# Kernel optimization log

Hardware: AMD Instinct MI355X
Metric: run time of the kernel (lower is better)

Reference implementation:

```python
import jax, jax.numpy as jnp
import numpy as np

N = 14           # num_wires
DEPTH = 2        # feature_map_depth; circuit applies DEPTH+1 StronglyEntanglingLayers blocks
SEL_LAYERS = 2   # params (B, 2*N*3) -> weights (B, 2, N, 3)


def _apply_1q(psi, U, w):
    # psi: (B, 2**N) complex64, U: (B,2,2) complex64, acts on wire w (wire 0 = MSB)
    B = psi.shape[0]
    psi = psi.reshape(B, 2 ** w, 2, -1)
    psi = jnp.einsum('bij,bajc->baic', U, psi)
    return psi.reshape(B, -1)


def _apply_cnot(psi, c, t):
    B = psi.shape[0]
    x = psi.reshape((B,) + (2,) * N)
    ca, ta = 1 + c, 1 + t
    a0 = jax.lax.index_in_dim(x, 0, ca, keepdims=True)
    a1 = jnp.flip(jax.lax.index_in_dim(x, 1, ca, keepdims=True), axis=ta)
    return jnp.concatenate([a0, a1], axis=ca).reshape(B, -1)


def _expz(psi, w):
    # <Z_w> = P(bit_w = 0) - P(bit_w = 1)
    B = psi.shape[0]
    p = (psi.real ** 2 + psi.imag ** 2).reshape(B, 2 ** w, 2, -1)
    return p[:, :, 0].sum(axis=(1, 2)) - p[:, :, 1].sum(axis=(1, 2))


def _rot(phi, theta, omega):
    # PennyLane Rot = RZ(omega) RY(theta) RZ(phi); returns (B,2,2) complex
    c, s = jnp.cos(theta / 2), jnp.sin(theta / 2)
    u00 = jnp.exp(-0.5j * (phi + omega)) * c
    u01 = -jnp.exp(0.5j * (phi - omega)) * s
    u10 = jnp.exp(-0.5j * (phi - omega)) * s
    u11 = jnp.exp(0.5j * (phi + omega)) * c
    return jnp.stack([jnp.stack([u00, u01], -1), jnp.stack([u10, u11], -1)], -2)


def _circuit(phases, weights):
    # phases: (B, N) float32, weights: (B, SEL_LAYERS, N, 3) float32
    B = phases.shape[0]
    psi = jnp.zeros((B, 2 ** N), jnp.complex64).at[:, 0].set(1.0)
    # AngleEmbedding (rotation='X'): RX(phi_w) on each wire
    for w in range(N):
        th = phases[:, w] / 2
        c, s = jnp.cos(th), jnp.sin(th)
        U = jnp.stack([jnp.stack([c + 0j, -1j * s], -1),
                       jnp.stack([-1j * s, c + 0j], -1)], -2)
        psi = _apply_1q(psi, U.astype(jnp.complex64), w)
    # (feature_map_depth + 1) StronglyEntanglingLayers blocks, all sharing `weights`
    for _ in range(DEPTH + 1):
        for l in range(SEL_LAYERS):
            for w in range(N):
                U = _rot(weights[:, l, w, 0], weights[:, l, w, 1], weights[:, l, w, 2])
                psi = _apply_1q(psi, U.astype(jnp.complex64), w)
            r = (l % (N - 1)) + 1  # PennyLane default ranges
            for w in range(N):
                psi = _apply_cnot(psi, w, (w + r) % N)
    return jnp.stack([_expz(psi, w) for w in range(N)], axis=1)  # (B, N)


def setup_inputs() -> dict:
    key = jax.random.key(0)
    k1, k2, k3, k4 = jax.random.split(key, 4)
    B = 512
    return {
        'state_batch': jax.random.normal(k1, (B, 2 ** N, 2), jnp.float32),
        'params': jax.random.normal(k2, (B, SEL_LAYERS * N * 3), jnp.float32),
        'head_w': jax.random.normal(k3, (1, N), jnp.float32) / np.float32(np.sqrt(N)),
        'head_b': jax.random.normal(k4, (1,), jnp.float32),
    }


def reference(state_batch, params, head_w, head_b):
    B = state_batch.shape[0]
    # torch.angle of a real tensor: pi where negative, 0 otherwise
    phases = jnp.where(state_batch.reshape(B, -1) < 0,
                       jnp.float32(np.pi), jnp.float32(0.0))[:, :N]
    weights = params.reshape(B, SEL_LAYERS, N, 3)
    qmeas = _circuit(phases, weights)            # (B, N)
    return (qmeas @ head_w.T + head_b)[:, 0]     # (B,)
```

## Files before the change

### kernel.cpp

```cpp
#include <hip/hip_runtime.h>


#define NW 14
#define NSTATE (1 << NW)
#define NTHREADS 1024
#define STATE_SLOTS (NSTATE + ((NSTATE >> 6) << 1))

__device__ __forceinline__ int SLOT(int i) { return i + ((i >> 6) << 1); }

typedef float v2f __attribute__((ext_vector_type(2)));

__device__ __forceinline__ float2 cmul(float2 a, float2 b) {
    return make_float2(a.x * b.x - a.y * b.y, a.x * b.y + a.y * b.x);
}

__device__ __forceinline__ v2f pk_mul_bl(v2f a, v2f b) {
    v2f d;
    asm("v_pk_mul_f32 %0, %1, %2 op_sel:[0,0] op_sel_hi:[1,0]"
        : "=v"(d) : "v"(a), "v"(b));
    return d;
}
__device__ __forceinline__ v2f pk_fma_bl(v2f a, v2f b, v2f c) {
    v2f d;
    asm("v_pk_fma_f32 %0, %1, %2, %3 op_sel:[0,0,0] op_sel_hi:[1,0,1]"
        : "=v"(d) : "v"(a), "v"(b), "v"(c));
    return d;
}
__device__ __forceinline__ v2f pk_fma_sw(v2f a, v2f b, v2f c) {
    v2f d;
    asm("v_pk_fma_f32 %0, %1, %2, %3 op_sel:[1,0,0] op_sel_hi:[0,1,1]"
        : "=v"(d) : "v"(a), "v"(b), "v"(c));
    return d;
}

struct RingConsts { unsigned col[2][NW]; unsigned flow[2][16]; };
constexpr RingConsts make_rc() {
    RingConsts rc{};
    for (int ri = 0; ri < 2; ++ri) {
        for (int bb = 0; bb < NW; ++bb) {
            unsigned x = 1u << bb;
            for (int w = 0; w < NW; ++w) {
                int pc = 13 - w, pt = 13 - ((w + ri + 1) % NW);
                x ^= ((x >> pc) & 1u) << pt;
            }
            rc.col[ri][bb] = x;
        }
        for (int k = 0; k < 16; ++k) {
            unsigned x = 0;
            for (int b = 0; b < 4; ++b) if ((k >> b) & 1) x ^= rc.col[ri][b];
            rc.flow[ri][k] = x;
        }
    }
    return rc;
}
constexpr RingConsts RC = make_rc();

#define GSTAGE(W) \
    const float4 g0 = G4[(W)*4+0], g1 = G4[(W)*4+1], \
                 g2 = G4[(W)*4+2], g3 = G4[(W)*4+3]; \
    const v2f U00 = (v2f){g0.x,g0.y}, V00 = (v2f){g0.z,g0.w}; \
    const v2f U01 = (v2f){g1.x,g1.y}, V01 = (v2f){g1.z,g1.w}; \
    const v2f U10 = (v2f){g2.x,g2.y}, V10 = (v2f){g2.z,g2.w}; \
    const v2f U11 = (v2f){g3.x,g3.y}, V11 = (v2f){g3.z,g3.w};

#define CBFA(X, Y) { \
    v2f n0 = pk_mul_bl(X, U00); n0 = pk_fma_sw(X, V00, n0); \
    n0 = pk_fma_bl(Y, U01, n0); n0 = pk_fma_sw(Y, V01, n0); \
    v2f n1 = pk_mul_bl(X, U10); n1 = pk_fma_sw(X, V10, n1); \
    n1 = pk_fma_bl(Y, U11, n1); n1 = pk_fma_sw(Y, V11, n1); \
    X = n0; Y = n1; }

template<int LO>
__device__ __forceinline__ void rot_pass(float2* st_, const float4* G4, int t)
{
    constexpr int S = (1 << LO) + ((LO >= 6) ? (1 << (LO - 5)) : 0);
    const int lowmask = (1 << LO) - 1;
    const int base = ((t >> LO) << (LO + 4)) | (t & lowmask);
    float2* p = st_ + SLOT(base);
    float2* q = p + 8 * S;
    v2f A0  = *(const v2f*)(p + 0*S), A1  = *(const v2f*)(p + 1*S),
        A2  = *(const v2f*)(p + 2*S), A3  = *(const v2f*)(p + 3*S),
        A4  = *(const v2f*)(p + 4*S), A5  = *(const v2f*)(p + 5*S),
        A6  = *(const v2f*)(p + 6*S), A7  = *(const v2f*)(p + 7*S),
        A8  = *(const v2f*)(q + 0*S), A9  = *(const v2f*)(q + 1*S),
        A10 = *(const v2f*)(q + 2*S), A11 = *(const v2f*)(q + 3*S),
        A12 = *(const v2f*)(q + 4*S), A13 = *(const v2f*)(q + 5*S),
        A14 = *(const v2f*)(q + 6*S), A15 = *(const v2f*)(q + 7*S);
    { GSTAGE(13 - LO - 3)
      CBFA(A0,A8) CBFA(A1,A9) CBFA(A2,A10) CBFA(A3,A11)
      CBFA(A4,A12) CBFA(A5,A13) CBFA(A6,A14) CBFA(A7,A15) }
    { GSTAGE(13 - LO - 2)
      CBFA(A0,A4) CBFA(A1,A5) CBFA(A2,A6) CBFA(A3,A7)
      CBFA(A8,A12) CBFA(A9,A13) CBFA(A10,A14) CBFA(A11,A15) }
    { GSTAGE(13 - LO - 1)
      CBFA(A0,A2) CBFA(A1,A3) CBFA(A4,A6) CBFA(A5,A7)
      CBFA(A8,A10) CBFA(A9,A11) CBFA(A12,A14) CBFA(A13,A15) }
    { GSTAGE(13 - LO)
      CBFA(A0,A1) CBFA(A2,A3) CBFA(A4,A5) CBFA(A6,A7)
      CBFA(A8,A9) CBFA(A10,A11) CBFA(A12,A13) CBFA(A14,A15) }
    *(v2f*)(p + 0*S) = A0;  *(v2f*)(p + 1*S) = A1;
    *(v2f*)(p + 2*S) = A2;  *(v2f*)(p + 3*S) = A3;
    *(v2f*)(p + 4*S) = A4;  *(v2f*)(p + 5*S) = A5;
    *(v2f*)(p + 6*S) = A6;  *(v2f*)(p + 7*S) = A7;
    *(v2f*)(q + 0*S) = A8;  *(v2f*)(q + 1*S) = A9;
    *(v2f*)(q + 2*S) = A10; *(v2f*)(q + 3*S) = A11;
    *(v2f*)(q + 4*S) = A12; *(v2f*)(q + 5*S) = A13;
    *(v2f*)(q + 6*S) = A14; *(v2f*)(q + 7*S) = A15;
}

#define LOW_LOAD_GATES \
    float2* pc = st_ + SLOT(t << 4); \
    const float4* lp = (const float4*)pc; \
    const float4 r0 = lp[0], r1 = lp[1], r2 = lp[2], r3 = lp[3], \
                 r4 = lp[4], r5 = lp[5], r6 = lp[6], r7 = lp[7]; \
    v2f A0  = (v2f){r0.x,r0.y}, A1  = (v2f){r0.z,r0.w}, \
        A2  = (v2f){r1.x,r1.y}, A3  = (v2f){r1.z,r1.w}, \
        A4  = (v2f){r2.x,r2.y}, A5  = (v2f){r2.z,r2.w}, \
        A6  = (v2f){r3.x,r3.y}, A7  = (v2f){r3.z,r3.w}, \
        A8  = (v2f){r4.x,r4.y}, A9  = (v2f){r4.z,r4.w}, \
        A10 = (v2f){r5.x,r5.y}, A11 = (v2f){r5.z,r5.w}, \
        A12 = (v2f){r6.x,r6.y}, A13 = (v2f){r6.z,r6.w}, \
        A14 = (v2f){r7.x,r7.y}, A15 = (v2f){r7.z,r7.w}; \
    { GSTAGE(12) \
      CBFA(A0,A2) CBFA(A1,A3) CBFA(A4,A6) CBFA(A5,A7) \
      CBFA(A8,A10) CBFA(A9,A11) CBFA(A12,A14) CBFA(A13,A15) } \
    { GSTAGE(13) \
      CBFA(A0,A1) CBFA(A2,A3) CBFA(A4,A5) CBFA(A6,A7) \
      CBFA(A8,A9) CBFA(A10,A11) CBFA(A12,A13) CBFA(A14,A15) }

template<int RI>
__device__ __forceinline__ void rot_low_ring(float2* st_, const float4* G4, int t,
                                             const unsigned* lutA_, const unsigned* lutB_)
{
    LOW_LOAD_GATES
    const unsigned fb = lutA_[t & 31] ^ lutB_[t >> 5];
    __syncthreads();
#define SCT(k, Ak) st_[SLOT((int)(fb ^ RC.flow[RI][k]))] = make_float2(Ak.x, Ak.y);
    SCT(0,A0) SCT(1,A1) SCT(2,A2) SCT(3,A3) SCT(4,A4) SCT(5,A5) SCT(6,A6) SCT(7,A7)
    SCT(8,A8) SCT(9,A9) SCT(10,A10) SCT(11,A11) SCT(12,A12) SCT(13,A13) SCT(14,A14) SCT(15,A15)
#undef SCT
}

__device__ __forceinline__ float rot_low_meas(float2* st_, const float4* G4, int t,
                                              const unsigned* lutA_, const unsigned* lutB_,
                                              const float* s_hw)
{
    LOW_LOAD_GATES
    const unsigned fb = lutA_[t & 31] ^ lutB_[t >> 5];
#define SGV(b) ((((fb >> b) & 1u) ? -1.f : 1.f) * s_hw[13 - (b)])
    const float sg0 = SGV(0),  sg1 = SGV(1),  sg2 = SGV(2),  sg3 = SGV(3),
                sg4 = SGV(4),  sg5 = SGV(5),  sg6 = SGV(6),  sg7 = SGV(7),
                sg8 = SGV(8),  sg9 = SGV(9),  sg10 = SGV(10), sg11 = SGV(11),
                sg12 = SGV(12), sg13 = SGV(13);
#undef SGV
    const float chiS = ((sg0 + sg1) + (sg2 + sg3)) + ((sg4 + sg5) + (sg6 + sg7))
                     + ((sg8 + sg9) + (sg10 + sg11)) + (sg12 + sg13);
#define SUBSUM(F) ( ((F)&1u?sg0:0.f) + ((F)&2u?sg1:0.f) + ((F)&4u?sg2:0.f) + ((F)&8u?sg3:0.f) \
                  + ((F)&16u?sg4:0.f) + ((F)&32u?sg5:0.f) + ((F)&64u?sg6:0.f) + ((F)&128u?sg7:0.f) \
                  + ((F)&256u?sg8:0.f) + ((F)&512u?sg9:0.f) + ((F)&1024u?sg10:0.f) + ((F)&2048u?sg11:0.f) \
                  + ((F)&4096u?sg12:0.f) + ((F)&8192u?sg13:0.f) )
    float acc = 0.f;
#define MEASA(k, Ak) { const float p2 = fmaf(Ak.x, Ak.x, Ak.y * Ak.y); \
    acc = fmaf(p2, chiS - 2.f * SUBSUM(RC.flow[1][k]), acc); }
    MEASA(0,A0) MEASA(1,A1) MEASA(2,A2) MEASA(3,A3)
    MEASA(4,A4) MEASA(5,A5) MEASA(6,A6) MEASA(7,A7)
    MEASA(8,A8) MEASA(9,A9) MEASA(10,A10) MEASA(11,A11)
    MEASA(12,A12) MEASA(13,A13) MEASA(14,A14) MEASA(15,A15)
#undef MEASA
#undef SUBSUM
    return acc;
}

__global__ __launch_bounds__(NTHREADS)
__attribute__((amdgpu_waves_per_eu(4, 4)))
void qsim(const float* __restrict__ sb, const float* __restrict__ pr,
          const float* __restrict__ hw, const float* __restrict__ hb,
          float* __restrict__ out)
{
    __shared__ __align__(16) float2 st[STATE_SLOTS];
    __shared__ __align__(16) float4 rotc[2][NW * 4];
    __shared__ unsigned lutA[2][32], lutB[2][32];
    __shared__ float s_hw[NW];
    __shared__ float s_red[NTHREADS / 64];
    __shared__ unsigned s_bmask;

    const int bid = blockIdx.x;
    const int t = threadIdx.x;

    if (t < 28) {
        int l = t / NW, w = t % NW;
        const float* p = pr + bid * 84 + l * 42 + w * 3;
        float phi = p[0], th = p[1], om = p[2];
        float s, cth;  __sincosf(0.5f * th, &s, &cth);
        float sa, ca, sd, cd;
        __sincosf(0.5f * (phi + om), &sa, &ca);
        __sincosf(0.5f * (phi - om), &sd, &cd);
        const float u00x = ca * cth, u00y = -sa * cth;
        const float u01x = -cd * s,  u01y = -sd * s;
        const float u10x = cd * s,   u10y = -sd * s;
        const float u11x = ca * cth, u11y = sa * cth;
        rotc[l][w*4+0] = make_float4(u00x, u00y, -u00y, u00y);
        rotc[l][w*4+1] = make_float4(u01x, u01y, -u01y, u01y);
        rotc[l][w*4+2] = make_float4(u10x, u10y, -u10y, u10y);
        rotc[l][w*4+3] = make_float4(u11x, u11y, -u11y, u11y);
    }
    if (t >= 64 && t < 192) {
        int j = t - 64, ri = j >> 6, tb = (j >> 5) & 1, m = j & 31;
        unsigned x = 0;
        for (int b = 0; b < 5; ++b)
            if ((m >> b) & 1) x ^= RC.col[ri][(tb ? 9 : 4) + b];
        if (tb) lutB[ri][m] = x; else lutA[ri][m] = x;
    }
    if (t >= 192 && t < 206) s_hw[t - 192] = hw[t - 192];
    if (t == 224) {
        const float* row = sb + (size_t)bid * (NSTATE * 2);
        unsigned m = 0;
        for (int w = 0; w < NW; ++w) m |= (row[w] < 0.0f ? 1u : 0u) << (13 - w);
        s_bmask = m;
    }
    __syncthreads();

    {
        const unsigned bm = s_bmask;
        float2 ph = make_float2(1.f, 0.f);
#pragma unroll
        for (int w = 0; w < 10; ++w) {
            int v = (t >> (9 - w)) & 1;
            int bw = (bm >> (13 - w)) & 1;
            float4 e = rotc[0][w*4 + v*2 + bw];
            ph = cmul(ph, make_float2(e.x, e.y));
        }
        const unsigned fb = lutA[0][t & 31] ^ lutB[0][t >> 5];
#pragma unroll
        for (int k = 0; k < 16; ++k) {
            float4 e3 = rotc[0][10*4 + (((k >> 3) & 1) * 2) + ((bm >> 3) & 1)];
            float4 e2 = rotc[0][11*4 + (((k >> 2) & 1) * 2) + ((bm >> 2) & 1)];
            float4 e1 = rotc[0][12*4 + (((k >> 1) & 1) * 2) + ((bm >> 1) & 1)];
            float4 e0 = rotc[0][13*4 + ((k & 1) * 2) + (bm & 1)];
            float2 pl = cmul(cmul(make_float2(e3.x, e3.y), make_float2(e2.x, e2.y)),
                             cmul(make_float2(e1.x, e1.y), make_float2(e0.x, e0.y)));
            st[SLOT((int)(fb ^ RC.flow[0][k]))] = cmul(ph, pl);
        }
    }
    __syncthreads();

#pragma unroll 1
    for (int rep = 0; rep < 4; ++rep) {
        const int l = (rep & 1) ? 0 : 1;
        const float4* G4 = &rotc[l][0];
        rot_pass<10>(st, G4, t); __syncthreads();
        rot_pass<6>(st, G4, t);  __syncthreads();
        rot_pass<2>(st, G4, t);  __syncthreads();
        if (l) rot_low_ring<1>(st, G4, t, lutA[1], lutB[1]);
        else   rot_low_ring<0>(st, G4, t, lutA[0], lutB[0]);
        __syncthreads();
    }
    rot_pass<10>(st, &rotc[1][0], t); __syncthreads();
    rot_pass<6>(st, &rotc[1][0], t); __syncthreads();
    rot_pass<2>(st, &rotc[1][0], t); __syncthreads();
    float acc = rot_low_meas(st, &rotc[1][0], t, lutA[1], lutB[1], s_hw);

    for (int off = 32; off > 0; off >>= 1) acc += __shfl_down(acc, off);
    if ((t & 63) == 0) s_red[t >> 6] = acc;
    __syncthreads();
    if (t == 0) {
        float tot = 0.f;
#pragma unroll
        for (int i = 0; i < NTHREADS / 64; ++i) tot += s_red[i];
        out[bid] = tot + hb[0];
    }
}

extern "C" void kernel_launch(void* const* d_in, const int* in_sizes, int n_in,
                              void* d_out, int out_size, void* d_ws, size_t ws_size,
                              hipStream_t stream)
{
    const float* sb = (const float*)d_in[0];
    const float* pr = (const float*)d_in[1];
    const float* hw = (const float*)d_in[2];
    const float* hb = (const float*)d_in[3];
    float* out = (float*)d_out;
    const int B = in_sizes[1] / 84;
    qsim<<<B, NTHREADS, 0, stream>>>(sb, pr, hw, hb, out);
}
```

Measured before the change: 208.9 us.

## Process 32 amplitudes per thread with 512 threads to cut LDS passes

After: 196.6 us. 5.9% less time.

```diff
diff --git a/kernel.cpp b/kernel.cpp
--- a/kernel.cpp
+++ b/kernel.cpp
@@ -3,10 +3,8 @@
 
 #define NW 14
 #define NSTATE (1 << NW)
-#define NTHREADS 1024
+#define NTHREADS 512
 #define STATE_SLOTS (NSTATE + ((NSTATE >> 6) << 1))
-
-__device__ __forceinline__ int SLOT(int i) { return i + ((i >> 6) << 1); }
 
 typedef float v2f __attribute__((ext_vector_type(2)));
 
@@ -15,25 +13,19 @@
 }
 
 __device__ __forceinline__ v2f pk_mul_bl(v2f a, v2f b) {
-    v2f d;
-    asm("v_pk_mul_f32 %0, %1, %2 op_sel:[0,0] op_sel_hi:[1,0]"
-        : "=v"(d) : "v"(a), "v"(b));
-    return d;
+    v2f d; asm("v_pk_mul_f32 %0, %1, %2 op_sel:[0,0] op_sel_hi:[1,0]"
+               : "=v"(d) : "v"(a), "v"(b)); return d;
 }
 __device__ __forceinline__ v2f pk_fma_bl(v2f a, v2f b, v2f c) {
-    v2f d;
-    asm("v_pk_fma_f32 %0, %1, %2, %3 op_sel:[0,0,0] op_sel_hi:[1,0,1]"
-        : "=v"(d) : "v"(a), "v"(b), "v"(c));
-    return d;
+    v2f d; asm("v_pk_fma_f32 %0, %1, %2, %3 op_sel:[0,0,0] op_sel_hi:[1,0,1]"
+               : "=v"(d) : "v"(a), "v"(b), "v"(c)); return d;
 }
 __device__ __forceinline__ v2f pk_fma_sw(v2f a, v2f b, v2f c) {
-    v2f d;
-    asm("v_pk_fma_f32 %0, %1, %2, %3 op_sel:[1,0,0] op_sel_hi:[0,1,1]"
-        : "=v"(d) : "v"(a), "v"(b), "v"(c));
-    return d;
-}
-
-struct RingConsts { unsigned col[2][NW]; unsigned flow[2][16]; };
+    v2f d; asm("v_pk_fma_f32 %0, %1, %2, %3 op_sel:[1,0,0] op_sel_hi:[0,1,1]"
+               : "=v"(d) : "v"(a), "v"(b), "v"(c)); return d;
+}
+
+struct RingConsts { unsigned col[2][NW]; unsigned flow[2][32]; };
 constexpr RingConsts make_rc() {
     RingConsts rc{};
     for (int ri = 0; ri < 2; ++ri) {
@@ -45,9 +37,9 @@
             }
             rc.col[ri][bb] = x;
         }
-        for (int k = 0; k < 16; ++k) {
+        for (int k = 0; k < 32; ++k) {
             unsigned x = 0;
-            for (int b = 0; b < 4; ++b) if ((k >> b) & 1) x ^= rc.col[ri][b];
+            for (int b = 0; b < 5; ++b) if ((k >> b) & 1) x ^= rc.col[ri][b];
             rc.flow[ri][k] = x;
         }
     }
@@ -70,83 +62,93 @@
     n1 = pk_fma_bl(Y, U11, n1); n1 = pk_fma_sw(Y, V11, n1); \
     X = n0; Y = n1; }
 
-template<int LO>
-__device__ __forceinline__ void rot_pass(float2* st_, const float4* G4, int t)
-{
-    constexpr int S = (1 << LO) + ((LO >= 6) ? (1 << (LO - 5)) : 0);
-    const int lowmask = (1 << LO) - 1;
-    const int base = ((t >> LO) << (LO + 4)) | (t & lowmask);
-    float2* p = st_ + SLOT(base);
-    float2* q = p + 8 * S;
-    v2f A0  = *(const v2f*)(p + 0*S), A1  = *(const v2f*)(p + 1*S),
-        A2  = *(const v2f*)(p + 2*S), A3  = *(const v2f*)(p + 3*S),
-        A4  = *(const v2f*)(p + 4*S), A5  = *(const v2f*)(p + 5*S),
-        A6  = *(const v2f*)(p + 6*S), A7  = *(const v2f*)(p + 7*S),
-        A8  = *(const v2f*)(q + 0*S), A9  = *(const v2f*)(q + 1*S),
-        A10 = *(const v2f*)(q + 2*S), A11 = *(const v2f*)(q + 3*S),
-        A12 = *(const v2f*)(q + 4*S), A13 = *(const v2f*)(q + 5*S),
-        A14 = *(const v2f*)(q + 6*S), A15 = *(const v2f*)(q + 7*S);
-    { GSTAGE(13 - LO - 3)
-      CBFA(A0,A8) CBFA(A1,A9) CBFA(A2,A10) CBFA(A3,A11)
-      CBFA(A4,A12) CBFA(A5,A13) CBFA(A6,A14) CBFA(A7,A15) }
-    { GSTAGE(13 - LO - 2)
-      CBFA(A0,A4) CBFA(A1,A5) CBFA(A2,A6) CBFA(A3,A7)
-      CBFA(A8,A12) CBFA(A9,A13) CBFA(A10,A14) CBFA(A11,A15) }
-    { GSTAGE(13 - LO - 1)
-      CBFA(A0,A2) CBFA(A1,A3) CBFA(A4,A6) CBFA(A5,A7)
-      CBFA(A8,A10) CBFA(A9,A11) CBFA(A12,A14) CBFA(A13,A15) }
-    { GSTAGE(13 - LO)
-      CBFA(A0,A1) CBFA(A2,A3) CBFA(A4,A5) CBFA(A6,A7)
-      CBFA(A8,A9) CBFA(A10,A11) CBFA(A12,A13) CBFA(A14,A15) }
-    *(v2f*)(p + 0*S) = A0;  *(v2f*)(p + 1*S) = A1;
-    *(v2f*)(p + 2*S) = A2;  *(v2f*)(p + 3*S) = A3;
-    *(v2f*)(p + 4*S) = A4;  *(v2f*)(p + 5*S) = A5;
-    *(v2f*)(p + 6*S) = A6;  *(v2f*)(p + 7*S) = A7;
-    *(v2f*)(q + 0*S) = A8;  *(v2f*)(q + 1*S) = A9;
-    *(v2f*)(q + 2*S) = A10; *(v2f*)(q + 3*S) = A11;
-    *(v2f*)(q + 4*S) = A12; *(v2f*)(q + 5*S) = A13;
-    *(v2f*)(q + 6*S) = A14; *(v2f*)(q + 7*S) = A15;
+#define FE32(M) M(0) M(1) M(2) M(3) M(4) M(5) M(6) M(7) M(8) M(9) M(10) M(11) \
+    M(12) M(13) M(14) M(15) M(16) M(17) M(18) M(19) M(20) M(21) M(22) M(23) \
+    M(24) M(25) M(26) M(27) M(28) M(29) M(30) M(31)
+
+#define P4(M) M(A0,A16) M(A1,A17) M(A2,A18) M(A3,A19) M(A4,A20) M(A5,A21) M(A6,A22) M(A7,A23) \
+              M(A8,A24) M(A9,A25) M(A10,A26) M(A11,A27) M(A12,A28) M(A13,A29) M(A14,A30) M(A15,A31)
+#define P3(M) M(A0,A8) M(A1,A9) M(A2,A10) M(A3,A11) M(A4,A12) M(A5,A13) M(A6,A14) M(A7,A15) \
+              M(A16,A24) M(A17,A25) M(A18,A26) M(A19,A27) M(A20,A28) M(A21,A29) M(A22,A30) M(A23,A31)
+#define P2(M) M(A0,A4) M(A1,A5) M(A2,A6) M(A3,A7) M(A8,A12) M(A9,A13) M(A10,A14) M(A11,A15) \
+              M(A16,A20) M(A17,A21) M(A18,A22) M(A19,A23) M(A24,A28) M(A25,A29) M(A26,A30) M(A27,A31)
+#define P1(M) M(A0,A2) M(A1,A3) M(A4,A6) M(A5,A7) M(A8,A10) M(A9,A11) M(A12,A14) M(A13,A15) \
+              M(A16,A18) M(A17,A19) M(A20,A22) M(A21,A23) M(A24,A26) M(A25,A27) M(A28,A30) M(A29,A31)
+#define P0(M) M(A0,A1) M(A2,A3) M(A4,A5) M(A6,A7) M(A8,A9) M(A10,A11) M(A12,A13) M(A14,A15) \
+              M(A16,A17) M(A18,A19) M(A20,A21) M(A22,A23) M(A24,A25) M(A26,A27) M(A28,A29) M(A30,A31)
+
+template<int LO, int W0>
+__device__ __forceinline__ void rot_pass5(float2* st_, const float4* G4, int t)
+{
+    const int base = ((t >> LO) << (LO + 5)) | (t & ((1 << LO) - 1));
+    float2* pA = st_ + (base + ((base >> 6) << 1));
+#define OFF(k) ((((k)) << LO) + (((((k)) << LO) >> 6) << 1))
+    float2* pB = pA + OFF(16);
+#define ADR(k) ((k) < 16 ? (pA + OFF(k)) : (pB + OFF((k) - 16)))
+#define DECL(k) v2f A##k;
+    FE32(DECL)
+#undef DECL
+#define LD(k) A##k = *(const v2f*)ADR(k);
+    FE32(LD)
+#undef LD
+    { GSTAGE(W0+0) P4(CBFA) }
+    { GSTAGE(W0+1) P3(CBFA) }
+    { GSTAGE(W0+2) P2(CBFA) }
+    { GSTAGE(W0+3) P1(CBFA) }
+    { GSTAGE(W0+4) P0(CBFA) }
+#define ST(k) *(v2f*)ADR(k) = A##k;
+    FE32(ST)
+#undef ST
+#undef ADR
+#undef OFF
 }
 
 #define LOW_LOAD_GATES \
-    float2* pc = st_ + SLOT(t << 4); \
-    const float4* lp = (const float4*)pc; \
-    const float4 r0 = lp[0], r1 = lp[1], r2 = lp[2], r3 = lp[3], \
-                 r4 = lp[4], r5 = lp[5], r6 = lp[6], r7 = lp[7]; \
-    v2f A0  = (v2f){r0.x,r0.y}, A1  = (v2f){r0.z,r0.w}, \
-        A2  = (v2f){r1.x,r1.y}, A3  = (v2f){r1.z,r1.w}, \
-        A4  = (v2f){r2.x,r2.y}, A5  = (v2f){r2.z,r2.w}, \
-        A6  = (v2f){r3.x,r3.y}, A7  = (v2f){r3.z,r3.w}, \
-        A8  = (v2f){r4.x,r4.y}, A9  = (v2f){r4.z,r4.w}, \
-        A10 = (v2f){r5.x,r5.y}, A11 = (v2f){r5.z,r5.w}, \
-        A12 = (v2f){r6.x,r6.y}, A13 = (v2f){r6.z,r6.w}, \
-        A14 = (v2f){r7.x,r7.y}, A15 = (v2f){r7.z,r7.w}; \
-    { GSTAGE(12) \
-      CBFA(A0,A2) CBFA(A1,A3) CBFA(A4,A6) CBFA(A5,A7) \
-      CBFA(A8,A10) CBFA(A9,A11) CBFA(A12,A14) CBFA(A13,A15) } \
-    { GSTAGE(13) \
-      CBFA(A0,A1) CBFA(A2,A3) CBFA(A4,A5) CBFA(A6,A7) \
-      CBFA(A8,A9) CBFA(A10,A11) CBFA(A12,A13) CBFA(A14,A15) }
+    const float4* lp = (const float4*)(st_ + (32 * t + ((t >> 1) << 1))); \
+    const float4 q0 = lp[0],  q1 = lp[1],  q2 = lp[2],  q3 = lp[3], \
+                 q4 = lp[4],  q5 = lp[5],  q6 = lp[6],  q7 = lp[7], \
+                 q8 = lp[8],  q9 = lp[9],  q10 = lp[10], q11 = lp[11], \
+                 q12 = lp[12], q13 = lp[13], q14 = lp[14], q15 = lp[15]; \
+    v2f A0  = (v2f){q0.x,q0.y},  A1  = (v2f){q0.z,q0.w}, \
+        A2  = (v2f){q1.x,q1.y},  A3  = (v2f){q1.z,q1.w}, \
+        A4  = (v2f){q2.x,q2.y},  A5  = (v2f){q2.z,q2.w}, \
+        A6  = (v2f){q3.x,q3.y},  A7  = (v2f){q3.z,q3.w}, \
+        A8  = (v2f){q4.x,q4.y},  A9  = (v2f){q4.z,q4.w}, \
+        A10 = (v2f){q5.x,q5.y},  A11 = (v2f){q5.z,q5.w}, \
+        A12 = (v2f){q6.x,q6.y},  A13 = (v2f){q6.z,q6.w}, \
+        A14 = (v2f){q7.x,q7.y},  A15 = (v2f){q7.z,q7.w}, \
+        A16 = (v2f){q8.x,q8.y},  A17 = (v2f){q8.z,q8.w}, \
+        A18 = (v2f){q9.x,q9.y},  A19 = (v2f){q9.z,q9.w}, \
+        A20 = (v2f){q10.x,q10.y}, A21 = (v2f){q10.z,q10.w}, \
+        A22 = (v2f){q11.x,q11.y}, A23 = (v2f){q11.z,q11.w}, \
+        A24 = (v2f){q12.x,q12.y}, A25 = (v2f){q12.z,q12.w}, \
+        A26 = (v2f){q13.x,q13.y}, A27 = (v2f){q13.z,q13.w}, \
+        A28 = (v2f){q14.x,q14.y}, A29 = (v2f){q14.z,q14.w}, \
+        A30 = (v2f){q15.x,q15.y}, A31 = (v2f){q15.z,q15.w}; \
+    { GSTAGE(10) P3(CBFA) } \
+    { GSTAGE(11) P2(CBFA) } \
+    { GSTAGE(12) P1(CBFA) } \
+    { GSTAGE(13) P0(CBFA) }
 
 template<int RI>
-__device__ __forceinline__ void rot_low_ring(float2* st_, const float4* G4, int t,
-                                             const unsigned* lutA_, const unsigned* lutB_)
+__device__ __forceinline__ void rot_low_ring5(float2* st_, const float4* G4, int t,
+                                              const unsigned* lA, const unsigned* lB)
 {
     LOW_LOAD_GATES
-    const unsigned fb = lutA_[t & 31] ^ lutB_[t >> 5];
-    __syncthreads();
-#define SCT(k, Ak) st_[SLOT((int)(fb ^ RC.flow[RI][k]))] = make_float2(Ak.x, Ak.y);
-    SCT(0,A0) SCT(1,A1) SCT(2,A2) SCT(3,A3) SCT(4,A4) SCT(5,A5) SCT(6,A6) SCT(7,A7)
-    SCT(8,A8) SCT(9,A9) SCT(10,A10) SCT(11,A11) SCT(12,A12) SCT(13,A13) SCT(14,A14) SCT(15,A15)
-#undef SCT
-}
-
-__device__ __forceinline__ float rot_low_meas(float2* st_, const float4* G4, int t,
-                                              const unsigned* lutA_, const unsigned* lutB_,
-                                              const float* s_hw)
+    const unsigned fb = lA[t & 31] ^ lB[t >> 5];
+    __syncthreads();
+#define SC(k) { const unsigned ix = fb ^ RC.flow[RI][(k)]; \
+    st_[ix + ((ix >> 6) << 1)] = make_float2(A##k.x, A##k.y); }
+    FE32(SC)
+#undef SC
+}
+
+__device__ __forceinline__ float rot_low_meas5(float2* st_, const float4* G4, int t,
+                                               const unsigned* lA, const unsigned* lB,
+                                               const float* s_hw)
 {
     LOW_LOAD_GATES
-    const unsigned fb = lutA_[t & 31] ^ lutB_[t >> 5];
+    const unsigned fb = lA[t & 31] ^ lB[t >> 5];
 #define SGV(b) ((((fb >> b) & 1u) ? -1.f : 1.f) * s_hw[13 - (b)])
     const float sg0 = SGV(0),  sg1 = SGV(1),  sg2 = SGV(2),  sg3 = SGV(3),
                 sg4 = SGV(4),  sg5 = SGV(5),  sg6 = SGV(6),  sg7 = SGV(7),
@@ -160,26 +162,23 @@
                   + ((F)&256u?sg8:0.f) + ((F)&512u?sg9:0.f) + ((F)&1024u?sg10:0.f) + ((F)&2048u?sg11:0.f) \
                   + ((F)&4096u?sg12:0.f) + ((F)&8192u?sg13:0.f) )
     float acc = 0.f;
-#define MEASA(k, Ak) { const float p2 = fmaf(Ak.x, Ak.x, Ak.y * Ak.y); \
-    acc = fmaf(p2, chiS - 2.f * SUBSUM(RC.flow[1][k]), acc); }
-    MEASA(0,A0) MEASA(1,A1) MEASA(2,A2) MEASA(3,A3)
-    MEASA(4,A4) MEASA(5,A5) MEASA(6,A6) MEASA(7,A7)
-    MEASA(8,A8) MEASA(9,A9) MEASA(10,A10) MEASA(11,A11)
-    MEASA(12,A12) MEASA(13,A13) MEASA(14,A14) MEASA(15,A15)
-#undef MEASA
+#define MEASK(k) { const float p2 = fmaf(A##k.x, A##k.x, A##k.y * A##k.y); \
+    acc = fmaf(p2, chiS - 2.f * SUBSUM(RC.flow[1][(k)]), acc); }
+    FE32(MEASK)
+#undef MEASK
 #undef SUBSUM
     return acc;
 }
 
-__global__ __launch_bounds__(NTHREADS)
-__attribute__((amdgpu_waves_per_eu(4, 4)))
+__global__ __launch_bounds__(NTHREADS, 2)
 void qsim(const float* __restrict__ sb, const float* __restrict__ pr,
           const float* __restrict__ hw, const float* __restrict__ hb,
           float* __restrict__ out)
 {
     __shared__ __align__(16) float2 st[STATE_SLOTS];
     __shared__ __align__(16) float4 rotc[2][NW * 4];
-    __shared__ unsigned lutA[2][32], lutB[2][32];
+    __shared__ unsigned lutA[2][32], lutB[2][16];
+    __shared__ float2 low_tab[32];
     __shared__ float s_hw[NW];
     __shared__ float s_red[NTHREADS / 64];
     __shared__ unsigned s_bmask;
@@ -204,43 +203,55 @@
         rotc[l][w*4+2] = make_float4(u10x, u10y, -u10y, u10y);
         rotc[l][w*4+3] = make_float4(u11x, u11y, -u11y, u11y);
     }
-    if (t >= 64 && t < 192) {
-        int j = t - 64, ri = j >> 6, tb = (j >> 5) & 1, m = j & 31;
+    if (t >= 64 && t < 128) {
+        int j = t - 64, ri = j >> 5, m = j & 31;
         unsigned x = 0;
-        for (int b = 0; b < 5; ++b)
-            if ((m >> b) & 1) x ^= RC.col[ri][(tb ? 9 : 4) + b];
-        if (tb) lutB[ri][m] = x; else lutA[ri][m] = x;
-    }
-    if (t >= 192 && t < 206) s_hw[t - 192] = hw[t - 192];
-    if (t == 224) {
+        for (int b = 0; b < 5; ++b) if ((m >> b) & 1) x ^= RC.col[ri][5 + b];
+        lutA[ri][m] = x;
+    }
+    if (t >= 128 && t < 160) {
+        int j = t - 128, ri = j >> 4, m = j & 15;
+        unsigned x = 0;
+        for (int b = 0; b < 4; ++b) if ((m >> b) & 1) x ^= RC.col[ri][10 + b];
+        lutB[ri][m] = x;
+    }
+    if (t >= 160 && t < 174) s_hw[t - 160] = hw[t - 160];
+    if (t == 192) {
         const float* row = sb + (size_t)bid * (NSTATE * 2);
         unsigned m = 0;
         for (int w = 0; w < NW; ++w) m |= (row[w] < 0.0f ? 1u : 0u) << (13 - w);
         s_bmask = m;
     }
     __syncthreads();
+    if (t < 32) {
+        const unsigned bm = s_bmask;
+        float2 v = make_float2(1.f, 0.f);
+#pragma unroll
+        for (int b = 0; b < 5; ++b) {
+            int w = 13 - b, kb = (t >> b) & 1, cb = (bm >> b) & 1;
+            float4 e = rotc[0][w*4 + kb*2 + cb];
+            v = cmul(v, make_float2(e.x, e.y));
+        }
+        low_tab[t] = v;
+    }
+    __syncthreads();
 
     {
         const unsigned bm = s_bmask;
         float2 ph = make_float2(1.f, 0.f);
 #pragma unroll
-        for (int w = 0; w < 10; ++w) {
-            int v = (t >> (9 - w)) & 1;
+        for (int w = 0; w < 9; ++w) {
+            int v = (t >> (8 - w)) & 1;
             int bw = (bm >> (13 - w)) & 1;
             float4 e = rotc[0][w*4 + v*2 + bw];
             ph = cmul(ph, make_float2(e.x, e.y));
         }
         const unsigned fb = lutA[0][t & 31] ^ lutB[0][t >> 5];
-#pragma unroll
-        for (int k = 0; k < 16; ++k) {
-            float4 e3 = rotc[0][10*4 + (((k >> 3) & 1) * 2) + ((bm >> 3) & 1)];
-            float4 e2 = rotc[0][11*4 + (((k >> 2) & 1) * 2) + ((bm >> 2) & 1)];
-            float4 e1 = rotc[0][12*4 + (((k >> 1) & 1) * 2) + ((bm >> 1) & 1)];
-            float4 e0 = rotc[0][13*4 + ((k & 1) * 2) + (bm & 1)];
-            float2 pl = cmul(cmul(make_float2(e3.x, e3.y), make_float2(e2.x, e2.y)),
-                             cmul(make_float2(e1.x, e1.y), make_float2(e0.x, e0.y)));
-            st[SLOT((int)(fb ^ RC.flow[0][k]))] = cmul(ph, pl);
-        }
+#define INITK(k) { const unsigned ix = fb ^ RC.flow[0][(k)]; \
+    const float2 lt = low_tab[(k)]; \
+    st[ix + ((ix >> 6) << 1)] = cmul(ph, lt); }
+        FE32(INITK)
+#undef INITK
     }
     __syncthreads();
 
@@ -248,17 +259,15 @@
     for (int rep = 0; rep < 4; ++rep) {
         const int l = (rep & 1) ? 0 : 1;
         const float4* G4 = &rotc[l][0];
-        rot_pass<10>(st, G4, t); __syncthreads();
-        rot_pass<6>(st, G4, t);  __syncthreads();
-        rot_pass<2>(st, G4, t);  __syncthreads();
-        if (l) rot_low_ring<1>(st, G4, t, lutA[1], lutB[1]);
-        else   rot_low_ring<0>(st, G4, t, lutA[0], lutB[0]);
+        rot_pass5<9, 0>(st, G4, t); __syncthreads();
+        rot_pass5<4, 5>(st, G4, t); __syncthreads();
+        if (l) rot_low_ring5<1>(st, G4, t, lutA[1], lutB[1]);
+        else   rot_low_ring5<0>(st, G4, t, lutA[0], lutB[0]);
         __syncthreads();
     }
-    rot_pass<10>(st, &rotc[1][0], t); __syncthreads();
-    rot_pass<6>(st, &rotc[1][0], t); __syncthreads();
-    rot_pass<2>(st, &rotc[1][0], t); __syncthreads();
-    float acc = rot_low_meas(st, &rotc[1][0], t, lutA[1], lutB[1], s_hw);
+    rot_pass5<9, 0>(st, &rotc[1][0], t); __syncthreads();
+    rot_pass5<4, 5>(st, &rotc[1][0], t); __syncthreads();
+    float acc = rot_low_meas5(st, &rotc[1][0], t, lutA[1], lutB[1], s_hw);
 
     for (int off = 32; off > 0; off >>= 1) acc += __shfl_down(acc, off);
     if ((t & 63) == 0) s_red[t >> 6] = acc;
```
